# Kernel optimization log

Measured on AMD Instinct MI355X. Metric: run time of the kernel, lower is better.

Reference implementation:

```python
import jax, jax.numpy as jnp
import numpy as np

D_MODEL = 1024
NUM_HEADS = 16
DEPTH = D_MODEL // NUM_HEADS
B, S = 4, 2048


def setup_inputs() -> dict:
    key = jax.random.key(0)
    ks = jax.random.split(key, 12)
    s = 1.0 / np.sqrt(D_MODEL)
    return {
        "q": jax.random.normal(ks[0], (B, S, D_MODEL), jnp.float32),
        "k": jax.random.normal(ks[1], (B, S, D_MODEL), jnp.float32),
        "v": jax.random.normal(ks[2], (B, S, D_MODEL), jnp.float32),
        "mask": jax.random.randint(ks[3], (B, S), 0, 2, jnp.int32),
        "wq_w": jax.random.uniform(ks[4], (D_MODEL, D_MODEL), jnp.float32, -s, s),
        "wq_b": jnp.zeros((D_MODEL,), jnp.float32),
        "wk_w": jax.random.uniform(ks[5], (D_MODEL, D_MODEL), jnp.float32, -s, s),
        "wk_b": jnp.zeros((D_MODEL,), jnp.float32),
        "wv_w": jax.random.uniform(ks[6], (D_MODEL, D_MODEL), jnp.float32, -s, s),
        "wv_b": jnp.zeros((D_MODEL,), jnp.float32),
        "wo_w": jax.random.uniform(ks[7], (D_MODEL, D_MODEL), jnp.float32, -s, s),
        "wo_b": jnp.zeros((D_MODEL,), jnp.float32),
    }


def _split_heads(x):
    # [B, S, D] -> [B, H, S, depth]
    b, s, _ = x.shape
    return x.reshape(b, s, NUM_HEADS, DEPTH).transpose(0, 2, 1, 3)


def reference(q, k, v, mask, wq_w, wq_b, wk_w, wk_b, wv_w, wv_b, wo_w, wo_b):
    qh = _split_heads(q @ wq_w.T + wq_b)
    kh = _split_heads(k @ wk_w.T + wk_b)
    vh = _split_heads(v @ wv_w.T + wv_b)
    # [B, H, Sq, Sk]
    logits = jnp.einsum("bhqd,bhkd->bhqk", qh, kh) / jnp.sqrt(
        jnp.asarray(DEPTH, jnp.float32))
    # 2D mask -> [B, 1, 1, Sk], masked_fill where mask == 0
    m = mask[:, None, None, :]
    logits = jnp.where(m == 0, jnp.asarray(-1e9, logits.dtype), logits)
    attn = jax.nn.softmax(logits, axis=-1)
    out = jnp.einsum("bhqk,bhkd->bhqd", attn, vh)
    out = out.transpose(0, 2, 1, 3).reshape(q.shape[0], -1, D_MODEL)
    return out @ wo_w.T + wo_b
```

## Files before the change

kernel.cpp:

```cpp
#include <hip/hip_runtime.h>
#include <hip/hip_bf16.h>
#include <stdint.h>

typedef __bf16 bf16_t;
typedef __bf16 bf16x8 __attribute__((ext_vector_type(8)));
typedef __bf16 bf16x2 __attribute__((ext_vector_type(2)));
typedef float  f32x4  __attribute__((ext_vector_type(4)));
typedef float  f32x16 __attribute__((ext_vector_type(16)));
typedef unsigned int u32;
typedef u32 u32x4 __attribute__((ext_vector_type(4)));

#define D_MODEL 1024
#define NHEAD   16
#define DEPTH   64
#define BATCH   4
#define SEQ     2048
#define MROWS   (BATCH*SEQ)

#define SC 0.18033688011112042f

__device__ __forceinline__ void gload16(const void* g, void* l) {
    __builtin_amdgcn_global_load_lds(
        (__attribute__((address_space(1))) void*)(uintptr_t)g,
        (__attribute__((address_space(3))) void*)l,
        16, 0, 0);
}

__device__ __forceinline__ u32 pk2(float a, float b) {
    bf16x2 t; t[0] = (bf16_t)a; t[1] = (bf16_t)b;
    return __builtin_bit_cast(u32, t);
}

__global__ __launch_bounds__(256) void cvt3_kernel(const float* __restrict__ s0, bf16_t* __restrict__ d0,
                                                   const float* __restrict__ s1, bf16_t* __restrict__ d1,
                                                   const float* __restrict__ s2, bf16_t* __restrict__ d2,
                                                   int n8) {
    int i = blockIdx.x * 256 + threadIdx.x;
    if (i >= n8) return;
    const float* src; bf16_t* dst;
    switch (blockIdx.y) {
        case 0: src = s0; dst = d0; break;
        case 1: src = s1; dst = d1; break;
        default: src = s2; dst = d2; break;
    }
    const float4* s4 = (const float4*)src;
    float4 a = s4[2*(size_t)i], b = s4[2*(size_t)i + 1];
    bf16x8 o;
    o[0] = (bf16_t)a.x; o[1] = (bf16_t)a.y; o[2] = (bf16_t)a.z; o[3] = (bf16_t)a.w;
    o[4] = (bf16_t)b.x; o[5] = (bf16_t)b.y; o[6] = (bf16_t)b.z; o[7] = (bf16_t)b.w;
    *(bf16x8*)(dst + 8*(size_t)i) = o;
}

__global__ __launch_bounds__(256) void cvtw_kernel(const float* __restrict__ s0, bf16_t* __restrict__ d0,
                                                   const float* __restrict__ s1, bf16_t* __restrict__ d1,
                                                   const float* __restrict__ s2, bf16_t* __restrict__ d2,
                                                   const float* __restrict__ s3, bf16_t* __restrict__ d3,
                                                   int n8) {
    int i = blockIdx.x * 256 + threadIdx.x;
    if (i >= n8) return;
    const float* src; bf16_t* dst;
    switch (blockIdx.y) {
        case 0: src = s0; dst = d0; break;
        case 1: src = s1; dst = d1; break;
        case 2: src = s2; dst = d2; break;
        default: src = s3; dst = d3; break;
    }
    const float4* s4 = (const float4*)src;
    float4 a = s4[2*(size_t)i], b = s4[2*(size_t)i + 1];
    bf16x8 o;
    o[0] = (bf16_t)a.x; o[1] = (bf16_t)a.y; o[2] = (bf16_t)a.z; o[3] = (bf16_t)a.w;
    o[4] = (bf16_t)b.x; o[5] = (bf16_t)b.y; o[6] = (bf16_t)b.z; o[7] = (bf16_t)b.w;
    *(bf16x8*)(dst + 8*(size_t)i) = o;
}

template<int MODE>
__global__ __launch_bounds__(256) void gemm_bt(const bf16_t* __restrict__ A,
                                               const bf16_t* __restrict__ Bw,
                                               const float* __restrict__ bias,
                                               bf16_t* __restrict__ Cb,
                                               float* __restrict__ Cf,
                                               int M, int N, int K, float scale) {
    __shared__ bf16_t Smem[2*128*64];
    bf16_t* As = Smem;
    bf16_t* Bs = Smem + 128*64;
    const int tid  = threadIdx.x;
    const int wave = tid >> 6, lane = tid & 63;
    const int lr = lane & 15, lk = (lane >> 4) * 8;
    const int bm = (blockIdx.x >> 3) * 128, bn = (blockIdx.x & 7) * 128;
    const int wr = (wave >> 1) * 64, wc = (wave & 1) * 64;

    f32x4 acc[4][4] = {};

    for (int kt = 0; kt < K; kt += 64) {
#pragma unroll
        for (int p = 0; p < 4; ++p) {
            int chunk = p*256 + tid;
            int r  = chunk >> 3;
            int cs = ((chunk & 7) ^ (r & 7)) * 8;
            gload16(A  + (size_t)(bm + r)*K + kt + cs, As + (size_t)chunk*8);
            gload16(Bw + (size_t)(bn + r)*K + kt + cs, Bs + (size_t)chunk*8);
        }
        __syncthreads();
        const char* AsB = (const char*)As;
        const char* BsB = (const char*)Bs;
#pragma unroll
        for (int ks = 0; ks < 2; ++ks) {
            int kb = (ks*32 + lk) * 2;
            bf16x8 af[4], bfv[4];
#pragma unroll
            for (int mi = 0; mi < 4; ++mi) {
                int row = wr + mi*16 + lr;
                af[mi] = *(const bf16x8*)(AsB + ((row*128 + kb) ^ ((row & 7) << 4)));
            }
#pragma unroll
            for (int ni = 0; ni < 4; ++ni) {
                int row = wc + ni*16 + lr;
                bfv[ni] = *(const bf16x8*)(BsB + ((row*128 + kb) ^ ((row & 7) << 4)));
            }
            __builtin_amdgcn_s_setprio(1);
#pragma unroll
            for (int mi = 0; mi < 4; ++mi)
#pragma unroll
                for (int ni = 0; ni < 4; ++ni)
                    acc[mi][ni] = __builtin_amdgcn_mfma_f32_16x16x32_bf16(
                        af[mi], bfv[ni], acc[mi][ni], 0, 0, 0);
            __builtin_amdgcn_s_setprio(0);
        }
        __syncthreads();
    }

    if (MODE != 2) {
#pragma unroll
        for (int ni = 0; ni < 4; ++ni) {
            int col = bn + wc + ni*16 + lr;
            float bv = bias[col];
#pragma unroll
            for (int mi = 0; mi < 4; ++mi) {
#pragma unroll
                for (int j = 0; j < 4; ++j) {
                    int row = bm + wr + mi*16 + (lane >> 4)*4 + j;
                    float vv = (acc[mi][ni][j] + bv) * scale;
                    if (MODE == 1) Cb[(size_t)row*N + col] = (bf16_t)vv;
                    else           Cf[(size_t)row*N + col] = vv;
                }
            }
        }
    } else {
        char* TB = (char*)Smem;
#pragma unroll
        for (int ni = 0; ni < 4; ++ni) {
            int col = wc + ni*16 + lr;
            int swz = (col & 7) << 4;
            float bv = bias[bn + col];
#pragma unroll
            for (int mi = 0; mi < 4; ++mi)
#pragma unroll
                for (int j = 0; j < 4; ++j) {
                    int row = wr + mi*16 + (lane >> 4)*4 + j;
                    int sp  = (row & ~12) | ((row & 4) << 1) | ((row & 8) >> 1);
                    float vv = (acc[mi][ni][j] + bv) * scale;
                    *(bf16_t*)(TB + ((col*256 + sp*2) ^ swz)) = (bf16_t)vv;
                }
        }
        __syncthreads();
        const int b = bm >> 11, sl = bm & 2047;
#pragma unroll
        for (int p = 0; p < 8; ++p) {
            int id = p*256 + tid;
            int col = id >> 4, sg = id & 15;
            bf16x8 v8 = *(const bf16x8*)(TB + ((col*256 + sg*16) ^ ((col & 7) << 4)));
            int gc = bn + col;
            int bh = b*16 + (gc >> 6), d = gc & 63;
            *(bf16x8*)&Cb[((size_t)bh*DEPTH + d)*SEQ + sl + sg*8] = v8;
        }
    }
}

__global__ __launch_bounds__(256, 2) void attn_kernel(const bf16_t* __restrict__ Qp,
                                                      const bf16_t* __restrict__ Kp,
                                                      const bf16_t* __restrict__ Vt,
                                                      const int* __restrict__ mask,
                                                      bf16_t* __restrict__ AO) {
    __shared__ bf16_t Ks[3][64*64];
    __shared__ bf16_t Vs[3][64*64];
    __shared__ bf16_t mbias[SEQ];

    const int tid  = threadIdx.x;
    const int wave = tid >> 6, lane = tid & 63;
    const int lr5 = lane & 31;
    const int hi  = lane >> 5;

    const int flat = blockIdx.x + 8*blockIdx.y + 128*blockIdx.z;
    const int xcd = flat & 7, slot = flat >> 3;
    const int bh = xcd + 8*(slot >> 3);
    const int b = bh >> 4, h = bh & 15;
    const int q0 = (slot & 7) * 256;

    const size_t base  = (size_t)b * SEQ * D_MODEL + (size_t)h * DEPTH;
    const size_t vbase = (size_t)bh * DEPTH * SEQ;

    bf16x8 qf[2][4];
#pragma unroll
    for (int qs = 0; qs < 2; ++qs)
#pragma unroll
        for (int dc = 0; dc < 4; ++dc)
            qf[qs][dc] = *(const bf16x8*)&Qp[base +
                (size_t)(q0 + qs*128 + wave*32 + lr5)*D_MODEL + dc*16 + hi*8];

    u32x4 onew = {};
    onew[0] = hi ? 0u : 0x3F80u;
    const bf16x8 qone = __builtin_bit_cast(bf16x8, onew);

    {
        const int4* mp = (const int4*)&mask[(size_t)b*SEQ + tid*8];
        int4 m0 = mp[0], m1 = mp[1];
        bf16x8 mm;
        mm[0] = (m0.x == 0) ? (bf16_t)(-1e30f) : (bf16_t)0.0f;
        mm[1] = (m0.y == 0) ? (bf16_t)(-1e30f) : (bf16_t)0.0f;
        mm[2] = (m0.z == 0) ? (bf16_t)(-1e30f) : (bf16_t)0.0f;
        mm[3] = (m0.w == 0) ? (bf16_t)(-1e30f) : (bf16_t)0.0f;
        mm[4] = (m1.x == 0) ? (bf16_t)(-1e30f) : (bf16_t)0.0f;
        mm[5] = (m1.y == 0) ? (bf16_t)(-1e30f) : (bf16_t)0.0f;
        mm[6] = (m1.z == 0) ? (bf16_t)(-1e30f) : (bf16_t)0.0f;
        mm[7] = (m1.w == 0) ? (bf16_t)(-1e30f) : (bf16_t)0.0f;
        *(bf16x8*)&mbias[tid*8] = mm;
    }

    auto stage = [&](int t, int buf) {
#pragma unroll
        for (int p = 0; p < 2; ++p) {
            int chunk = p*256 + tid; int r = chunk >> 3;
            int cs = ((chunk & 7) ^ (r & 7)) * 8;
            gload16(Kp + base + (size_t)(t*64 + r)*D_MODEL + cs,
                    (bf16_t*)Ks[buf] + (size_t)chunk*8);
            gload16(Vt + vbase + (size_t)r*SEQ + t*64 + cs,
                    (bf16_t*)Vs[buf] + (size_t)chunk*8);
        }
    };

    f32x16 oA0 = {}, oA1 = {};
    f32x16 oB0 = {}, oB1 = {};
    float lA = 0.f, lB = 0.f;

    stage(0, 0); stage(1, 1); stage(2, 2);
    asm volatile("s_waitcnt vmcnt(8) lgkmcnt(0)");
    __builtin_amdgcn_s_barrier();

    int cb = 0;
    for (int t = 0; t < SEQ/64; ++t) {
        u32 mw0 = (u32)__builtin_bit_cast(unsigned short, mbias[t*64 + lr5]);
        u32 mw1 = (u32)__builtin_bit_cast(unsigned short, mbias[t*64 + 32 + lr5]);
        if (hi) { mw0 = 0; mw1 = 0; }
        u32x4 mv0 = {}, mv1 = {};
        mv0[0] = mw0; mv1[0] = mw1;
        bf16x8 afm0 = __builtin_bit_cast(bf16x8, mv0);
        bf16x8 afm1 = __builtin_bit_cast(bf16x8, mv1);

        const char* KsB = (const char*)Ks[cb];
        const char* VsB = (const char*)Vs[cb];

#pragma unroll
        for (int qs = 0; qs < 2; ++qs) {
            const f32x16 zz = {};
            f32x16 s0, s1;
            __builtin_amdgcn_s_setprio(1);
            s0 = __builtin_amdgcn_mfma_f32_32x32x16_bf16(afm0, qone, zz, 0, 0, 0);
            s1 = __builtin_amdgcn_mfma_f32_32x32x16_bf16(afm1, qone, zz, 0, 0, 0);
#pragma unroll
            for (int dc = 0; dc < 4; ++dc) {
                int colb = dc*32 + hi*16;
                int row0 = lr5, row1 = 32 + lr5;
                bf16x8 kf0 = *(const bf16x8*)(KsB + ((row0*128 + colb) ^ ((row0 & 7) << 4)));
                bf16x8 kf1 = *(const bf16x8*)(KsB + ((row1*128 + colb) ^ ((row1 & 7) << 4)));
                s0 = __builtin_amdgcn_mfma_f32_32x32x16_bf16(kf0, qf[qs][dc], s0, 0, 0, 0);
                s1 = __builtin_amdgcn_mfma_f32_32x32x16_bf16(kf1, qf[qs][dc], s1, 0, 0, 0);
            }
            __builtin_amdgcn_s_setprio(0);

            float lsum = 0.f;
#pragma unroll
            for (int kt = 0; kt < 2; ++kt) {
                const f32x16& sh = kt ? s1 : s0;
                float pv[16];
#pragma unroll
                for (int r = 0; r < 16; ++r) pv[r] = __builtin_exp2f(sh[r]);
                float su0 = 0.f, su1 = 0.f, su2 = 0.f, su3 = 0.f;
#pragma unroll
                for (int r = 0; r < 16; r += 4) {
                    su0 += pv[r]; su1 += pv[r+1]; su2 += pv[r+2]; su3 += pv[r+3];
                }
                lsum += (su0 + su1) + (su2 + su3);
#pragma unroll
                for (int c = 0; c < 2; ++c) {
                    u32x4 fwv;
#pragma unroll
                    for (int i = 0; i < 4; ++i)
                        fwv[i] = pk2(pv[c*8 + 2*i], pv[c*8 + 2*i + 1]);
                    bf16x8 pfrag = __builtin_bit_cast(bf16x8, fwv);
                    int colb = kt*64 + c*32 + hi*16;
                    int row0 = lr5, row1 = 32 + lr5;
                    bf16x8 vf0 = *(const bf16x8*)(VsB + ((row0*128 + colb) ^ ((row0 & 7) << 4)));
                    bf16x8 vf1 = *(const bf16x8*)(VsB + ((row1*128 + colb) ^ ((row1 & 7) << 4)));
                    __builtin_amdgcn_s_setprio(1);
                    if (qs == 0) {
                        oA0 = __builtin_amdgcn_mfma_f32_32x32x16_bf16(vf0, pfrag, oA0, 0, 0, 0);
                        oA1 = __builtin_amdgcn_mfma_f32_32x32x16_bf16(vf1, pfrag, oA1, 0, 0, 0);
                    } else {
                        oB0 = __builtin_amdgcn_mfma_f32_32x32x16_bf16(vf0, pfrag, oB0, 0, 0, 0);
                        oB1 = __builtin_amdgcn_mfma_f32_32x32x16_bf16(vf1, pfrag, oB1, 0, 0, 0);
                    }
                    __builtin_amdgcn_s_setprio(0);
                }
            }
            if (qs == 0) lA += lsum; else lB += lsum;
        }

        asm volatile("s_waitcnt vmcnt(4) lgkmcnt(0)");
        __builtin_amdgcn_s_barrier();
        if (t + 3 < SEQ/64) stage(t + 3, cb);
        ++cb; if (cb == 3) cb = 0;
    }

    char* TrB = (char*)Ks;
    const int qloc = wave*32 + lr5;
#pragma unroll
    for (int qs = 0; qs < 2; ++qs) {
        if (qs) __syncthreads();
        float lr_ = (qs == 0) ? lA : lB;
        float l_tot = lr_ + __shfl_xor(lr_, 32);
        float inv = 1.f / l_tot;
#pragma unroll
        for (int mt = 0; mt < 2; ++mt)
#pragma unroll
            for (int r = 0; r < 16; ++r) {
                int d = mt*32 + (r & 3) + 8*(r >> 2) + 4*hi;
                float val = (qs == 0 ? (mt ? oA1[r] : oA0[r])
                                     : (mt ? oB1[r] : oB0[r])) * inv;
                *(bf16_t*)(TrB + (qloc*128 + ((d*2) ^ ((qloc & 7) << 4)))) = (bf16_t)val;
            }
        __syncthreads();
#pragma unroll
        for (int p = 0; p < 4; ++p) {
            int id = p*256 + tid;
            int row = id >> 3, g = id & 7;
            bf16x8 v8 = *(const bf16x8*)(TrB + (row*128 + ((g*16) ^ ((row & 7) << 4))));
            *(bf16x8*)&AO[base + (size_t)(q0 + qs*128 + row)*D_MODEL + g*8] = v8;
        }
    }
}

extern "C" void kernel_launch(void* const* d_in, const int* in_sizes, int n_in,
                              void* d_out, int out_size, void* d_ws, size_t ws_size,
                              hipStream_t stream) {
    (void)in_sizes; (void)n_in; (void)out_size; (void)ws_size;
    const float* q    = (const float*)d_in[0];
    const float* k    = (const float*)d_in[1];
    const float* v    = (const float*)d_in[2];
    const int*   mask = (const int*)d_in[3];
    const float* wq_w = (const float*)d_in[4];
    const float* wq_b = (const float*)d_in[5];
    const float* wk_w = (const float*)d_in[6];
    const float* wk_b = (const float*)d_in[7];
    const float* wv_w = (const float*)d_in[8];
    const float* wv_b = (const float*)d_in[9];
    const float* wo_w = (const float*)d_in[10];
    const float* wo_b = (const float*)d_in[11];
    float* out = (float*)d_out;

    const size_t ACT = (size_t)MROWS * D_MODEL;
    const size_t WSZ = (size_t)D_MODEL * D_MODEL;
    bf16_t* B0 = (bf16_t*)d_ws;
    bf16_t* B1 = B0 + ACT;
    bf16_t* B2 = B1 + ACT;
    bf16_t* B3 = B2 + ACT;
    bf16_t* Wq = B3 + ACT;
    bf16_t* Wk = Wq + WSZ;
    bf16_t* Wv = Wk + WSZ;
    bf16_t* Wo = Wv + WSZ;

    const int wn8 = (int)(WSZ/8), an8 = (int)(ACT/8);
    cvtw_kernel<<<dim3(wn8/256, 4), dim3(256), 0, stream>>>(wq_w, Wq, wk_w, Wk, wv_w, Wv, wo_w, Wo, wn8);
    cvt3_kernel<<<dim3(an8/256, 3), dim3(256), 0, stream>>>(q, B0, k, B1, v, B2, an8);

    const int ggrid = (MROWS/128) * (D_MODEL/128);
    gemm_bt<1><<<ggrid, dim3(256), 0, stream>>>(B0, Wq, wq_b, B3, nullptr, MROWS, D_MODEL, D_MODEL, SC);
    gemm_bt<1><<<ggrid, dim3(256), 0, stream>>>(B1, Wk, wk_b, B0, nullptr, MROWS, D_MODEL, D_MODEL, 1.f);
    gemm_bt<2><<<ggrid, dim3(256), 0, stream>>>(B2, Wv, wv_b, B1, nullptr, MROWS, D_MODEL, D_MODEL, 1.f);

    attn_kernel<<<dim3(SEQ/256, NHEAD, BATCH), dim3(256), 0, stream>>>(B3, B0, B1, mask, B2);

    gemm_bt<0><<<ggrid, dim3(256), 0, stream>>>(B2, Wo, wo_b, nullptr, out, MROWS, D_MODEL, D_MODEL, 1.f);
}
```

Measured before the change: 229.0 us.

## Double-buffer GEMM LDS tiles with two-stage-ahead async global-to-LDS prefetch

Doubles the shared-memory allocation in the bf16 GEMM to hold two K-tiles and issues the global_load_lds for tile t+2 right after tile t is consumed. It uses explicit vmcnt waits and raw barriers instead of __syncthreads, so memory latency overlaps with MFMA work. The cost is 64KB of LDS per block, which may lower occupancy, plus reliance on hand-counted vmcnt values being correct.

```diff
diff --git a/kernel.cpp b/kernel.cpp
--- a/kernel.cpp
+++ b/kernel.cpp
@@ -80,29 +80,36 @@
                                                bf16_t* __restrict__ Cb,
                                                float* __restrict__ Cf,
                                                int M, int N, int K, float scale) {
-    __shared__ bf16_t Smem[2*128*64];
-    bf16_t* As = Smem;
-    bf16_t* Bs = Smem + 128*64;
+    __shared__ bf16_t Smem[4*128*64];
     const int tid  = threadIdx.x;
     const int wave = tid >> 6, lane = tid & 63;
     const int lr = lane & 15, lk = (lane >> 4) * 8;
     const int bm = (blockIdx.x >> 3) * 128, bn = (blockIdx.x & 7) * 128;
     const int wr = (wave >> 1) * 64, wc = (wave & 1) * 64;
 
-    f32x4 acc[4][4] = {};
-
-    for (int kt = 0; kt < K; kt += 64) {
+    auto stage = [&](int t, int buf) {
+        bf16_t* As = Smem + (size_t)buf * (2*128*64);
+        bf16_t* Bs = As + 128*64;
 #pragma unroll
         for (int p = 0; p < 4; ++p) {
             int chunk = p*256 + tid;
             int r  = chunk >> 3;
             int cs = ((chunk & 7) ^ (r & 7)) * 8;
-            gload16(A  + (size_t)(bm + r)*K + kt + cs, As + (size_t)chunk*8);
-            gload16(Bw + (size_t)(bn + r)*K + kt + cs, Bs + (size_t)chunk*8);
-        }
-        __syncthreads();
-        const char* AsB = (const char*)As;
-        const char* BsB = (const char*)Bs;
+            gload16(A  + (size_t)(bm + r)*K + t*64 + cs, As + (size_t)chunk*8);
+            gload16(Bw + (size_t)(bn + r)*K + t*64 + cs, Bs + (size_t)chunk*8);
+        }
+    };
+
+    f32x4 acc[4][4] = {};
+    const int NT = K / 64;
+
+    stage(0, 0); stage(1, 1);
+    asm volatile("s_waitcnt vmcnt(8)");
+    __builtin_amdgcn_s_barrier();
+
+    for (int t = 0; t < NT; ++t) {
+        const char* AsB = (const char*)(Smem + (size_t)(t & 1) * (2*128*64));
+        const char* BsB = AsB + 128*64*2;
 #pragma unroll
         for (int ks = 0; ks < 2; ++ks) {
             int kb = (ks*32 + lk) * 2;
@@ -126,7 +133,14 @@
                         af[mi], bfv[ni], acc[mi][ni], 0, 0, 0);
             __builtin_amdgcn_s_setprio(0);
         }
-        __syncthreads();
+        __builtin_amdgcn_s_barrier();
+        if (t + 2 < NT) {
+            stage(t + 2, t & 1);
+            asm volatile("s_waitcnt vmcnt(8)");
+        } else {
+            asm volatile("s_waitcnt vmcnt(0)");
+        }
+        __builtin_amdgcn_s_barrier();
     }
 
     if (MODE != 2) {
```

After: 234.2 us. +2.3%, slower.
